# Performance work log

Hardware: AMD Instinct MI355X
Metric: run time of the kernel (lower is better)

Reference implementation:

```python
import jax, jax.numpy as jnp
import numpy as np

# Model constants (match init_kwargs)
HIDDEN = 4096
N_HEADS = 32
N_KV_HEADS = 4
N_GROUPS = N_HEADS // N_KV_HEADS  # 8
QK_DIM = 192
V_DIM = 128
ROT_DIM = 64  # int(192 * 0.334), even
ROPE_THETA = 5000000.0


def rotate_half(x):
    x1, x2 = x[..., : x.shape[-1] // 2], x[..., x.shape[-1] // 2 :]
    return jnp.concatenate((-x2, x1), axis=-1)


def rope_cos_sin(position_ids):
    # position_ids: [B, S] int -> cos/sin: [B, S, ROT_DIM]
    inv_freq = 1.0 / (ROPE_THETA ** (jnp.arange(0, ROT_DIM, 2, dtype=jnp.float32) / ROT_DIM))
    freqs = position_ids.astype(jnp.float32)[:, :, None] * inv_freq[None, None, :]  # [B,S,ROT/2]
    emb = jnp.concatenate((freqs, freqs), axis=-1)  # [B,S,ROT]
    return jnp.cos(emb), jnp.sin(emb)


def setup_inputs() -> dict:
    key = jax.random.key(0)
    ks = jax.random.split(key, 6)
    B, S = 2, 2048
    hidden_states = jax.random.normal(ks[0], (B, S, HIDDEN), dtype=jnp.float32)
    # additive causal mask [B,1,S,S]
    causal = jnp.triu(jnp.full((S, S), -1e9, dtype=jnp.float32), k=1)
    attention_mask = jnp.broadcast_to(causal[None, None], (B, 1, S, S))
    position_ids = jnp.broadcast_to(jnp.arange(S, dtype=jnp.int64)[None], (B, S))
    scale = 0.02
    wq = jax.random.normal(ks[1], (N_HEADS * QK_DIM, HIDDEN), dtype=jnp.float32) * scale
    wk = jax.random.normal(ks[2], (N_KV_HEADS * QK_DIM, HIDDEN), dtype=jnp.float32) * scale
    wv = jax.random.normal(ks[3], (N_KV_HEADS * V_DIM, HIDDEN), dtype=jnp.float32) * scale
    wo = jax.random.normal(ks[4], (HIDDEN, N_HEADS * V_DIM), dtype=jnp.float32) * scale
    return {
        "hidden_states": hidden_states,
        "attention_mask": attention_mask,
        "position_ids": position_ids,
        "wq": wq,
        "wk": wk,
        "wv": wv,
        "wo": wo,
    }


def reference(hidden_states, attention_mask, position_ids, wq, wk, wv, wo):
    B, S, _ = hidden_states.shape
    # projections
    q = (hidden_states @ wq.T).reshape(B, S, N_HEADS, QK_DIM).transpose(0, 2, 1, 3)      # [B,H,S,Dq]
    k = (hidden_states @ wk.T).reshape(B, S, N_KV_HEADS, QK_DIM).transpose(0, 2, 1, 3)   # [B,Kh,S,Dq]
    v = (hidden_states @ wv.T).reshape(B, S, N_KV_HEADS, V_DIM).transpose(0, 2, 1, 3)    # [B,Kh,S,Dv]

    # partial RoPE on first ROT_DIM dims
    cos, sin = rope_cos_sin(position_ids)          # [B,S,ROT]
    cos, sin = cos[:, None], sin[:, None]          # [B,1,S,ROT]
    q_rot, q_pass = q[..., :ROT_DIM], q[..., ROT_DIM:]
    k_rot, k_pass = k[..., :ROT_DIM], k[..., ROT_DIM:]
    q_rot = q_rot * cos + rotate_half(q_rot) * sin
    k_rot = k_rot * cos + rotate_half(k_rot) * sin
    q = jnp.concatenate((q_rot, q_pass), axis=-1)
    k = jnp.concatenate((k_rot, k_pass), axis=-1)

    # GQA: group Q heads instead of materializing repeated K/V
    qg = q.reshape(B, N_KV_HEADS, N_GROUPS, S, QK_DIM)
    scores = jnp.einsum("bkgqd,bkld->bkgql", qg, k) / np.sqrt(QK_DIM).astype(np.float32)
    scores = scores + attention_mask[:, :, None]  # [B,1,1,S,S] broadcast
    probs = jax.nn.softmax(scores.astype(jnp.float32), axis=-1).astype(q.dtype)
    out = jnp.einsum("bkgql,bkld->bkgqd", probs, v)            # [B,Kh,G,S,Dv]
    out = out.reshape(B, N_HEADS, S, V_DIM).transpose(0, 2, 1, 3).reshape(B, S, N_HEADS * V_DIM)
    return out @ wo.T
```

## Files before the change

kernel.cpp:

```cpp
#include <hip/hip_runtime.h>
#include <hip/hip_bf16.h>

#define DEVI __device__ __forceinline__

typedef __attribute__((ext_vector_type(8))) short bf16x8;
typedef __attribute__((ext_vector_type(4))) short short4v;
typedef __attribute__((ext_vector_type(4))) float f32x4;

constexpr int S_LEN = 2048;
constexpr int NQKV  = 7424;
constexpr int KOFF  = 6144;
constexpr int VOFF  = 6912;
constexpr float SCALE = 0.07216878364870322f;
constexpr float LOG2E = 1.4426950408889634f;

DEVI short f2bf(float f) {
    union { __hip_bfloat16 h; short s; } u;
    u.h = __float2bfloat16(f);
    return u.s;
}
DEVI float bf2f(short b) {
    union { __hip_bfloat16 h; short s; } u;
    u.s = b;
    return __bfloat162float(u.h);
}

__global__ __launch_bounds__(256) void cvt_f32_bf16(const float4* __restrict__ src,
                                                    short* __restrict__ dst) {
    int i = blockIdx.x * 256 + threadIdx.x;
    float4 v = src[i];
    short4v o;
    o.x = f2bf(v.x); o.y = f2bf(v.y); o.z = f2bf(v.z); o.w = f2bf(v.w);
    *(short4v*)(dst + (size_t)i * 4) = o;
}

__global__ __launch_bounds__(256) void cvt_wcat(const float* __restrict__ wq,
                                                const float* __restrict__ wk,
                                                const float* __restrict__ wv,
                                                short* __restrict__ dst) {
    size_t i4 = (size_t)blockIdx.x * 256 + threadIdx.x;
    size_t e  = i4 * 4;
    size_t row = e >> 12;
    const float* s;
    if (row < 6144)      s = wq + e;
    else if (row < 6912) s = wk + (e - 25165824ull);
    else                 s = wv + (e - 28311552ull);
    float4 v = *(const float4*)s;
    short4v o;
    o.x = f2bf(v.x); o.y = f2bf(v.y); o.z = f2bf(v.z); o.w = f2bf(v.w);
    *(short4v*)(dst + e) = o;
}

__global__ __launch_bounds__(256) void rope_tab_k(float* __restrict__ tab) {
    int idx = blockIdx.x * 256 + threadIdx.x;
    int s = idx >> 5, i = idx & 31;
    float inv = powf(5.0e6f, -(float)i / 32.0f);
    float f = (float)s * inv;
    float sn, cs;
    sincosf(f, &sn, &cs);
    tab[(s << 6) + i]      = cs;
    tab[(s << 6) + 32 + i] = sn;
}

__global__ __launch_bounds__(256) void rope_apply(short* __restrict__ qkv,
                                                  const float* __restrict__ tab) {
    int idx  = blockIdx.x * 256 + threadIdx.x;
    int i    = idx & 31;
    int rest = idx >> 5;
    int u    = rest % 36;
    int tkn  = rest / 36;
    int s    = tkn & (S_LEN - 1);
    int col  = (u < 32) ? (u * 192 + i) : (KOFF + (u - 32) * 192 + i);
    short* p = qkv + (size_t)tkn * NQKV + col;
    float x1 = bf2f(p[0]), x2 = bf2f(p[32]);
    float c  = tab[(s << 6) + i];
    float sn = tab[(s << 6) + 32 + i];
    p[0]  = f2bf(x1 * c - x2 * sn);
    p[32] = f2bf(x2 * c + x1 * sn);
}

#define GLOAD16(gp, lp) __builtin_amdgcn_global_load_lds( \
    (const __attribute__((address_space(1))) void*)(gp),  \
    (__attribute__((address_space(3))) void*)(lp), 16, 0, 0)

DEVI void storeC(short* p, float v) { *p = f2bf(v); }
DEVI void storeC(float* p, float v) { *p = v; }

template <typename CT>
__global__ __launch_bounds__(256) void gemm_bt(const short* __restrict__ A,
                                               const short* __restrict__ B,
                                               CT* __restrict__ C,
                                               int K, int lda, int ldb, int ldc) {
    __shared__ short As[128 * 32];
    __shared__ short Bs[128 * 32];
    const int t    = threadIdx.x;
    const int lane = t & 63, wid = t >> 6;
    const int m0 = blockIdx.y * 128, n0 = blockIdx.x * 128;
    const int wm = (wid >> 1) * 64, wn = (wid & 1) * 64;
    const int rl = lane & 15;
    const int ko = (lane >> 4) * 8;

    f32x4 acc[4][4] = {};

    const int sr = lane >> 2;
    const int scol = (lane & 3) * 8;
    const short* ga = A + (size_t)(m0 + wid * 32 + sr) * lda + scol;
    const short* gb = B + (size_t)(n0 + wid * 32 + sr) * ldb + scol;
    short* la = As + wid * 1024;
    short* lb = Bs + wid * 1024;

    for (int kb = 0; kb < K; kb += 32) {
        GLOAD16(ga + kb,                      la);
        GLOAD16(ga + kb + (size_t)16 * lda,   la + 512);
        GLOAD16(gb + kb,                      lb);
        GLOAD16(gb + kb + (size_t)16 * ldb,   lb + 512);
        __syncthreads();
        bf16x8 af[4], bf[4];
#pragma unroll
        for (int mf = 0; mf < 4; ++mf)
            af[mf] = *(const bf16x8*)(As + (wm + mf * 16 + rl) * 32 + ko);
#pragma unroll
        for (int nf = 0; nf < 4; ++nf)
            bf[nf] = *(const bf16x8*)(Bs + (wn + nf * 16 + rl) * 32 + ko);
#pragma unroll
        for (int mf = 0; mf < 4; ++mf)
#pragma unroll
            for (int nf = 0; nf < 4; ++nf)
                acc[mf][nf] = __builtin_amdgcn_mfma_f32_16x16x32_bf16(
                    af[mf], bf[nf], acc[mf][nf], 0, 0, 0);
        __syncthreads();
    }
#pragma unroll
    for (int mf = 0; mf < 4; ++mf)
#pragma unroll
        for (int i = 0; i < 4; ++i) {
            size_t row = (size_t)(m0 + wm + mf * 16 + (lane >> 4) * 4 + i);
#pragma unroll
            for (int nf = 0; nf < 4; ++nf) {
                int col = n0 + wn + nf * 16 + rl;
                storeC(&C[row * ldc + col], acc[mf][nf][i]);
            }
        }
}

__global__ __launch_bounds__(256) void attn_fwd(const short* __restrict__ qkv,
                                                short* __restrict__ o) {
    const int qt  = blockIdx.x;
    const int bh  = blockIdx.y;
    const int b   = bh >> 5, h = bh & 31;
    const int kvh = h >> 3;
    const int t = threadIdx.x, lane = t & 63, w = t >> 6;
    const int rl = lane & 15, hi = lane >> 4;
    const int ko = hi * 8;

    __shared__ short Ks[64 * 200];
    __shared__ short Vt[128 * 72];
    __shared__ short Ps[4 * 16 * 72];

    bf16x8 qf[6];
    {
        const size_t qrow = (size_t)(b * S_LEN + qt * 64 + w * 16 + rl);
        const short* qp = qkv + qrow * NQKV + h * 192;
#pragma unroll
        for (int kk = 0; kk < 6; ++kk) qf[kk] = *(const bf16x8*)(qp + kk * 32 + ko);
    }

    f32x4 acc_o[8] = {};
    float m_run[4], l_run[4];
#pragma unroll
    for (int i = 0; i < 4; ++i) { m_run[i] = -3.0e38f; l_run[i] = 0.0f; }

    for (int kt = 0; kt <= qt; ++kt) {
        __syncthreads();
        const size_t krow0 = (size_t)(b * S_LEN + kt * 64);
#pragma unroll
        for (int c = 0; c < 6; ++c) {
            int ch = t + c * 256;
            int r = ch / 24, cc = ch % 24;
            bf16x8 v = *(const bf16x8*)(qkv + (krow0 + r) * NQKV + KOFF + kvh * 192 + cc * 8);
            *(bf16x8*)(Ks + r * 200 + cc * 8) = v;
        }
#pragma unroll
        for (int c = 0; c < 4; ++c) {
            int ch = t + c * 256;
            int r = ch & 63, cc = ch >> 6;
            bf16x8 v = *(const bf16x8*)(qkv + (krow0 + r) * NQKV + VOFF + kvh * 128 + cc * 8);
#pragma unroll
            for (int j = 0; j < 8; ++j) Vt[(cc * 8 + j) * 72 + r] = v[j];
        }
        __syncthreads();

        f32x4 sc4[4] = {};
#pragma unroll
        for (int kk = 0; kk < 6; ++kk) {
#pragma unroll
            for (int kf = 0; kf < 4; ++kf) {
                bf16x8 bfr = *(const bf16x8*)(Ks + (kf * 16 + rl) * 200 + kk * 32 + ko);
                sc4[kf] = __builtin_amdgcn_mfma_f32_16x16x32_bf16(qf[kk], bfr, sc4[kf], 0, 0, 0);
            }
        }

        const int q0   = qt * 64 + w * 16 + hi * 4;
        const int kcol = kt * 64 + rl;
#pragma unroll
        for (int kf = 0; kf < 4; ++kf)
#pragma unroll
            for (int i = 0; i < 4; ++i) {
                float s = sc4[kf][i] * SCALE;
                sc4[kf][i] = (kcol + kf * 16 > q0 + i) ? -3.0e38f : s;
            }

        float corr[4];
#pragma unroll
        for (int i = 0; i < 4; ++i) {
            float mx = fmaxf(fmaxf(sc4[0][i], sc4[1][i]), fmaxf(sc4[2][i], sc4[3][i]));
            mx = fmaxf(mx, __shfl_xor(mx, 1));
            mx = fmaxf(mx, __shfl_xor(mx, 2));
            mx = fmaxf(mx, __shfl_xor(mx, 4));
            mx = fmaxf(mx, __shfl_xor(mx, 8));
            float mnew = fmaxf(m_run[i], mx);
            float rs = 0.0f;
#pragma unroll
            for (int kf = 0; kf < 4; ++kf) {
                float p = exp2f((sc4[kf][i] - mnew) * LOG2E);
                sc4[kf][i] = p;
                rs += p;
            }
            rs += __shfl_xor(rs, 1);
            rs += __shfl_xor(rs, 2);
            rs += __shfl_xor(rs, 4);
            rs += __shfl_xor(rs, 8);
            float cr = exp2f((m_run[i] - mnew) * LOG2E);
            l_run[i] = l_run[i] * cr + rs;
            m_run[i] = mnew;
            corr[i]  = cr;
        }
#pragma unroll
        for (int vf = 0; vf < 8; ++vf)
#pragma unroll
            for (int i = 0; i < 4; ++i) acc_o[vf][i] *= corr[i];

        short* pw = Ps + w * (16 * 72);
#pragma unroll
        for (int kf = 0; kf < 4; ++kf)
#pragma unroll
            for (int i = 0; i < 4; ++i)
                pw[(hi * 4 + i) * 72 + kf * 16 + rl] = f2bf(sc4[kf][i]);

#pragma unroll
        for (int kk = 0; kk < 2; ++kk) {
            bf16x8 pa = *(const bf16x8*)(pw + rl * 72 + kk * 32 + ko);
#pragma unroll
            for (int vf = 0; vf < 8; ++vf) {
                bf16x8 vb = *(const bf16x8*)(Vt + (vf * 16 + rl) * 72 + kk * 32 + ko);
                acc_o[vf] = __builtin_amdgcn_mfma_f32_16x16x32_bf16(pa, vb, acc_o[vf], 0, 0, 0);
            }
        }
    }

    const size_t orow_base = (size_t)(b * S_LEN + qt * 64 + w * 16 + hi * 4);
#pragma unroll
    for (int i = 0; i < 4; ++i) {
        float inv = 1.0f / l_run[i];
        short* op = o + (orow_base + i) * 4096 + h * 128;
#pragma unroll
        for (int vf = 0; vf < 8; ++vf) op[vf * 16 + rl] = f2bf(acc_o[vf][i] * inv);
    }
}

extern "C" void kernel_launch(void* const* d_in, const int* in_sizes, int n_in,
                              void* d_out, int out_size, void* d_ws, size_t ws_size,
                              hipStream_t stream) {
    (void)in_sizes; (void)n_in; (void)out_size; (void)ws_size;
    const float* hs = (const float*)d_in[0];
    const float* wq = (const float*)d_in[3];
    const float* wk = (const float*)d_in[4];
    const float* wv = (const float*)d_in[5];
    const float* wo = (const float*)d_in[6];

    char*  ws   = (char*)d_ws;
    short* Xb   = (short*)ws;
    short* Wcat = (short*)(ws + 33554432ll);
    short* Ob   = Xb;
    short* Wob  = Wcat;
    short* qkv  = (short*)d_out;
    float* tab  = (float*)((char*)d_out + 60817408ll);
    float* outf = (float*)d_out;

    cvt_f32_bf16<<<16384, 256, 0, stream>>>((const float4*)hs, Xb);
    cvt_wcat<<<29696, 256, 0, stream>>>(wq, wk, wv, Wcat);
    dim3 g1(58, 32);
    gemm_bt<short><<<g1, 256, 0, stream>>>(Xb, Wcat, qkv, 4096, 4096, 4096, NQKV);
    rope_tab_k<<<256, 256, 0, stream>>>(tab);
    rope_apply<<<18432, 256, 0, stream>>>(qkv, tab);
    dim3 ga(32, 64);
    attn_fwd<<<ga, 256, 0, stream>>>(qkv, Ob);
    cvt_f32_bf16<<<16384, 256, 0, stream>>>((const float4*)wo, Wob);
    dim3 g2(32, 32);
    gemm_bt<float><<<g2, 256, 0, stream>>>(Ob, Wob, outf, 4096, 4096, 4096, 4096);
}
```

Measured before the change: 1.364 ms.

## Share K/V tiles across all GQA heads per block with double-buffered loads

```diff
diff --git a/kernel.cpp b/kernel.cpp
--- a/kernel.cpp
+++ b/kernel.cpp
@@ -143,71 +143,88 @@
         }
 }
 
-__global__ __launch_bounds__(256) void attn_fwd(const short* __restrict__ qkv,
-                                                short* __restrict__ o) {
+__global__ __launch_bounds__(512) void attn_fwd2(const short* __restrict__ qkv,
+                                                 short* __restrict__ o) {
     const int qt  = blockIdx.x;
-    const int bh  = blockIdx.y;
-    const int b   = bh >> 5, h = bh & 31;
-    const int kvh = h >> 3;
+    const int b   = blockIdx.y >> 2;
+    const int kvh = blockIdx.y & 3;
     const int t = threadIdx.x, lane = t & 63, w = t >> 6;
     const int rl = lane & 15, hi = lane >> 4;
     const int ko = hi * 8;
-
-    __shared__ short Ks[64 * 200];
-    __shared__ short Vt[128 * 72];
-    __shared__ short Ps[4 * 16 * 72];
+    const int h  = kvh * 8 + w;
+
+    __shared__ short Ks[2][64 * 200];
+    __shared__ short Vt[2][128 * 72];
+    __shared__ short Ps[8][16 * 72];
 
     bf16x8 qf[6];
     {
-        const size_t qrow = (size_t)(b * S_LEN + qt * 64 + w * 16 + rl);
+        const size_t qrow = (size_t)(b * S_LEN + qt * 16 + rl);
         const short* qp = qkv + qrow * NQKV + h * 192;
 #pragma unroll
         for (int kk = 0; kk < 6; ++kk) qf[kk] = *(const bf16x8*)(qp + kk * 32 + ko);
     }
 
+    int krow[3], kc8[3];
+#pragma unroll
+    for (int c = 0; c < 3; ++c) { int ch = t + c * 512; krow[c] = ch / 24; kc8[c] = ch % 24; }
+    const int r0 = (t & 31) * 2;
+    const int d0 = (t >> 5) * 8;
+    const short* kbase = qkv + (size_t)(b * S_LEN) * NQKV + KOFF + kvh * 192;
+    const short* vbase = qkv + (size_t)(b * S_LEN) * NQKV + VOFF + kvh * 128;
+
+    bf16x8 kreg0, kreg1, kreg2, vreg0, vreg1;
+    auto LOADT = [&](int kt) {
+        kreg0 = *(const bf16x8*)(kbase + (size_t)(kt * 64 + krow[0]) * NQKV + kc8[0] * 8);
+        kreg1 = *(const bf16x8*)(kbase + (size_t)(kt * 64 + krow[1]) * NQKV + kc8[1] * 8);
+        kreg2 = *(const bf16x8*)(kbase + (size_t)(kt * 64 + krow[2]) * NQKV + kc8[2] * 8);
+        vreg0 = *(const bf16x8*)(vbase + (size_t)(kt * 64 + r0)     * NQKV + d0);
+        vreg1 = *(const bf16x8*)(vbase + (size_t)(kt * 64 + r0 + 1) * NQKV + d0);
+    };
+    auto WRITET = [&](int bb) {
+        *(bf16x8*)(&Ks[bb][krow[0] * 200 + kc8[0] * 8]) = kreg0;
+        *(bf16x8*)(&Ks[bb][krow[1] * 200 + kc8[1] * 8]) = kreg1;
+        *(bf16x8*)(&Ks[bb][krow[2] * 200 + kc8[2] * 8]) = kreg2;
+#pragma unroll
+        for (int j = 0; j < 8; ++j) {
+            unsigned pk = (unsigned)(unsigned short)vreg0[j] |
+                          ((unsigned)(unsigned short)vreg1[j] << 16);
+            *(unsigned*)(&Vt[bb][(d0 + j) * 72 + r0]) = pk;
+        }
+    };
+
     f32x4 acc_o[8] = {};
     float m_run[4], l_run[4];
 #pragma unroll
     for (int i = 0; i < 4; ++i) { m_run[i] = -3.0e38f; l_run[i] = 0.0f; }
 
-    for (int kt = 0; kt <= qt; ++kt) {
+    const int nt = (qt >> 2) + 1;
+    LOADT(0);
+    WRITET(0);
+
+    for (int kt = 0; kt < nt; ++kt) {
         __syncthreads();
-        const size_t krow0 = (size_t)(b * S_LEN + kt * 64);
-#pragma unroll
-        for (int c = 0; c < 6; ++c) {
-            int ch = t + c * 256;
-            int r = ch / 24, cc = ch % 24;
-            bf16x8 v = *(const bf16x8*)(qkv + (krow0 + r) * NQKV + KOFF + kvh * 192 + cc * 8);
-            *(bf16x8*)(Ks + r * 200 + cc * 8) = v;
-        }
-#pragma unroll
-        for (int c = 0; c < 4; ++c) {
-            int ch = t + c * 256;
-            int r = ch & 63, cc = ch >> 6;
-            bf16x8 v = *(const bf16x8*)(qkv + (krow0 + r) * NQKV + VOFF + kvh * 128 + cc * 8);
-#pragma unroll
-            for (int j = 0; j < 8; ++j) Vt[(cc * 8 + j) * 72 + r] = v[j];
-        }
-        __syncthreads();
+        const int cur = kt & 1;
+        if (kt + 1 < nt) LOADT(kt + 1);
 
         f32x4 sc4[4] = {};
 #pragma unroll
         for (int kk = 0; kk < 6; ++kk) {
 #pragma unroll
             for (int kf = 0; kf < 4; ++kf) {
-                bf16x8 bfr = *(const bf16x8*)(Ks + (kf * 16 + rl) * 200 + kk * 32 + ko);
+                bf16x8 bfr = *(const bf16x8*)(&Ks[cur][(kf * 16 + rl) * 200 + kk * 32 + ko]);
                 sc4[kf] = __builtin_amdgcn_mfma_f32_16x16x32_bf16(qf[kk], bfr, sc4[kf], 0, 0, 0);
             }
         }
 
-        const int q0   = qt * 64 + w * 16 + hi * 4;
-        const int kcol = kt * 64 + rl;
+        const int q0 = qt * 16 + hi * 4;
+        const int kc = kt * 64 + rl;
 #pragma unroll
         for (int kf = 0; kf < 4; ++kf)
 #pragma unroll
             for (int i = 0; i < 4; ++i) {
                 float s = sc4[kf][i] * SCALE;
-                sc4[kf][i] = (kcol + kf * 16 > q0 + i) ? -3.0e38f : s;
+                sc4[kf][i] = (kc + kf * 16 > q0 + i) ? -3.0e38f : s;
             }
 
         float corr[4];
@@ -240,7 +257,7 @@
 #pragma unroll
             for (int i = 0; i < 4; ++i) acc_o[vf][i] *= corr[i];
 
-        short* pw = Ps + w * (16 * 72);
+        short* pw = &Ps[w][0];
 #pragma unroll
         for (int kf = 0; kf < 4; ++kf)
 #pragma unroll
@@ -252,13 +269,15 @@
             bf16x8 pa = *(const bf16x8*)(pw + rl * 72 + kk * 32 + ko);
 #pragma unroll
             for (int vf = 0; vf < 8; ++vf) {
-                bf16x8 vb = *(const bf16x8*)(Vt + (vf * 16 + rl) * 72 + kk * 32 + ko);
+                bf16x8 vb = *(const bf16x8*)(&Vt[cur][(vf * 16 + rl) * 72 + kk * 32 + ko]);
                 acc_o[vf] = __builtin_amdgcn_mfma_f32_16x16x32_bf16(pa, vb, acc_o[vf], 0, 0, 0);
             }
         }
+
+        if (kt + 1 < nt) WRITET((kt + 1) & 1);
     }
 
-    const size_t orow_base = (size_t)(b * S_LEN + qt * 64 + w * 16 + hi * 4);
+    const size_t orow_base = (size_t)(b * S_LEN + qt * 16 + hi * 4);
 #pragma unroll
     for (int i = 0; i < 4; ++i) {
         float inv = 1.0f / l_run[i];
@@ -293,8 +312,8 @@
     gemm_bt<short><<<g1, 256, 0, stream>>>(Xb, Wcat, qkv, 4096, 4096, 4096, NQKV);
     rope_tab_k<<<256, 256, 0, stream>>>(tab);
     rope_apply<<<18432, 256, 0, stream>>>(qkv, tab);
-    dim3 ga(32, 64);
-    attn_fwd<<<ga, 256, 0, stream>>>(qkv, Ob);
+    dim3 ga(128, 8);
+    attn_fwd2<<<ga, 512, 0, stream>>>(qkv, Ob);
     cvt_f32_bf16<<<16384, 256, 0, stream>>>((const float4*)wo, Wob);
     dim3 g2(32, 32);
     gemm_bt<float><<<g2, 256, 0, stream>>>(Ob, Wob, outf, 4096, 4096, 4096, 4096);
```

Result: faster. 1.167 ms (-14.4%).
